# Kernel optimization log

Hardware: AMD Instinct MI355X
Metric: run time of the kernel (lower is better)

## Reference

```python
import jax, jax.numpy as jnp
import numpy as np

LOG_STD_MAX = 2.0
LOG_STD_MIN = -5.0
N_LAYERS = 10
HID = 512
OBS = 21
ACT = 8
OVERALL = HID * (N_LAYERS + 1)          # 5632
IN_DIM = OBS + OVERALL                   # 5653
OUT_DIM = OVERALL + ACT                  # 5640
BATCH = 8192


def _block_banded_weight(rng):
    # staircase partitions, exactly as layer_init
    in_d = [0, OBS] + [OBS + HID * i for i in range(1, N_LAYERS + 2)]
    out_d = [0] + [HID * i for i in range(1, N_LAYERS + 2)] + [OUT_DIM]
    W = np.zeros((OUT_DIM, IN_DIM), dtype=np.float32)
    for i in range(N_LAYERS + 2):
        r0, r1 = out_d[i], out_d[i + 1]
        c0, c1 = in_d[i], in_d[i + 1]
        fan_in = c1 - c0
        std = np.sqrt(2.0 / fan_in)  # kaiming_normal_ fan_in, gain sqrt(2)
        W[r0:r1, c0:c1] = rng.standard_normal((r1 - r0, c1 - c0)).astype(np.float32) * std
    return jnp.asarray(W)


def setup_inputs() -> dict:
    key = jax.random.key(0)
    k1, k2, k3, k4, k5, k6 = jax.random.split(key, 6)
    rng = np.random.default_rng(0)
    return {
        "obs": jax.random.normal(k1, (BATCH, OBS), dtype=jnp.float32),
        "hidden0": jax.random.uniform(k2, (BATCH, OVERALL), dtype=jnp.float32),
        "prev_mean": jax.random.normal(k3, (BATCH, ACT), dtype=jnp.float32),
        "prev_logstd": jax.random.normal(k4, (BATCH, ACT), dtype=jnp.float32),
        "W_mean": _block_banded_weight(rng),
        "b_mean": jnp.zeros((OUT_DIM,), dtype=jnp.float32),
        "W_logstd": jax.random.normal(k5, (ACT, IN_DIM), dtype=jnp.float32) / np.sqrt(IN_DIM),
        "b_logstd": jax.random.normal(k6, (ACT,), dtype=jnp.float32) * 0.01,
    }


def reference(obs, hidden0, prev_mean, prev_logstd, W_mean, b_mean, W_logstd, b_logstd):
    x = jnp.concatenate([obs, hidden0], axis=1)            # [B, IN_DIM]
    new_x = x @ W_mean.T + b_mean                          # [B, OUT_DIM]
    new_hidden = jax.nn.relu(new_x[:, :-ACT])              # [B, OVERALL]
    new_mean = new_x[:, -ACT:]                             # [B, ACT]
    new_log_std = x @ W_logstd.T + b_logstd                # [B, ACT]
    # outputs come from the PREVIOUS step's (mean, log_std)
    log_std = jnp.tanh(prev_logstd)
    log_std = LOG_STD_MIN + 0.5 * (LOG_STD_MAX - LOG_STD_MIN) * (log_std + 1.0)
    return (prev_mean, log_std, new_hidden, new_mean, new_log_std)
```

## Files before the change

kernel.cpp:

```cpp
#include <hip/hip_runtime.h>
#include <math.h>

typedef unsigned short u16;
typedef unsigned int u32;
typedef __attribute__((ext_vector_type(8))) short short8;
typedef __attribute__((ext_vector_type(4))) float float4v;

#define BATCH   8192
#define OBS     21
#define HID     512
#define NL      10
#define OVERALL 5632
#define IN_DIM  5653
#define OUT_DIM 5640
#define ACT     8

#define O_PM   0
#define O_LS   65536
#define O_NH   131072
#define O_NM   (131072 + BATCH*OVERALL)
#define O_NLS  (O_NM + 65536)

#define WSP_TOTAL (10*512*512)
#define WSP_BYTES ((size_t)WSP_TOTAL * 2)

__device__ __forceinline__ u16 f2bf(float f) {
    u32 u = __float_as_uint(f);
    u32 r = (u + 0x7fffu + ((u >> 16) & 1u)) >> 16;
    return (u16)r;
}
__device__ __forceinline__ u32 pkbf(float a, float b) {
    return (u32)f2bf(a) | ((u32)f2bf(b) << 16);
}
__device__ __forceinline__ void gload_lds16(const void* g, void* l) {
    __builtin_amdgcn_global_load_lds(
        (const __attribute__((address_space(1))) char*)g,
        (__attribute__((address_space(3))) char*)l, 16, 0, 0);
}

__global__ __launch_bounds__(256) void k_pack(const float* __restrict__ Wm,
                                              u16* __restrict__ ws) {
    int idx = blockIdx.x * 256 + threadIdx.x;
    if (idx >= WSP_TOTAL) return;
    int z = idx >> 18;
    int rem = idx & 262143;
    int n = rem >> 9, k = rem & 511;
    float v = Wm[(size_t)(512 * (z + 1) + n) * IN_DIM + OBS + 512 * z + k];
    ws[idx] = f2bf(v);
}

#define BM 128
#define BN 128
#define BK 32
#define A_LD 40
__global__ __launch_bounds__(256, 2) void k_gemm(const float* __restrict__ X,
                                                 const float* __restrict__ Wm_raw,
                                                 const u16* __restrict__ Wp,
                                                 const float* __restrict__ b_mean,
                                                 float* __restrict__ out_h,
                                                 int packed) {
    __shared__ __attribute__((aligned(16))) u16 As[BM * A_LD];
    __shared__ __attribute__((aligned(16))) u16 Bs[BN * BK];
    int t = threadIdx.x;
    int wave = t >> 6, lane = t & 63;
    int quad = lane >> 4, r16 = lane & 15;
    int gm = blockIdx.x * BM;
    int gn = blockIdx.y * BN;
    int z = blockIdx.z;
    int wm = (wave >> 1) * 64;
    int wn = (wave & 1) * 64;
    int ar = t >> 1;
    int ah = t & 1;

    const float* Arow = X + (size_t)(gm + ar) * OVERALL + z * 512 + ah * 16;

    float4v acc[4][4];
#pragma unroll
    for (int i = 0; i < 4; i++)
#pragma unroll
        for (int j = 0; j < 4; j++) acc[i][j] = (float4v)0.f;

    for (int k0 = 0; k0 < 512; k0 += BK) {
        __syncthreads();
        {
            const float* ga = Arow + k0;
            float4 v0 = *(const float4*)(ga);
            float4 v1 = *(const float4*)(ga + 4);
            float4 v2 = *(const float4*)(ga + 8);
            float4 v3 = *(const float4*)(ga + 12);
            uint4 p0, p1;
            p0.x = pkbf(v0.x, v0.y); p0.y = pkbf(v0.z, v0.w);
            p0.z = pkbf(v1.x, v1.y); p0.w = pkbf(v1.z, v1.w);
            p1.x = pkbf(v2.x, v2.y); p1.y = pkbf(v2.z, v2.w);
            p1.z = pkbf(v3.x, v3.y); p1.w = pkbf(v3.z, v3.w);
            *(uint4*)&As[ar * A_LD + ah * 16] = p0;
            *(uint4*)&As[ar * A_LD + ah * 16 + 8] = p1;
        }
        if (packed) {
#pragma unroll
            for (int it = 0; it < 2; ++it) {
                int n = it * 64 + wave * 16 + (lane >> 2);
                int kk = (lane & 3) * 8;
                const u16* gb = Wp + (size_t)z * (512 * 512) + (size_t)(gn + n) * 512 + k0 + kk;
                gload_lds16(gb, (char*)Bs + it * 4096 + wave * 1024);
            }
        } else {
            int n = t >> 1, h = t & 1;
            const float* gb = Wm_raw + (size_t)(512 * (z + 1) + gn + n) * IN_DIM
                              + OBS + 512 * z + k0 + h * 16;
#pragma unroll
            for (int e = 0; e < 16; e += 2)
                *(u32*)&Bs[n * BK + h * 16 + e] = pkbf(gb[e], gb[e + 1]);
        }
        __syncthreads();

        short8 af[4], bf[4];
#pragma unroll
        for (int i = 0; i < 4; i++) {
            af[i] = *(const short8*)&As[(wm + i * 16 + r16) * A_LD + quad * 8];
            bf[i] = *(const short8*)&Bs[(wn + i * 16 + r16) * BK + quad * 8];
        }
#pragma unroll
        for (int i = 0; i < 4; i++)
#pragma unroll
            for (int j = 0; j < 4; j++)
                acc[i][j] = __builtin_amdgcn_mfma_f32_16x16x32_bf16(af[i], bf[j], acc[i][j], 0, 0, 0);
    }

    int colblock = 512 * (z + 1);
#pragma unroll
    for (int j = 0; j < 4; j++) {
        int n_loc = gn + wn + j * 16 + r16;
        float bias = b_mean[colblock + n_loc];
#pragma unroll
        for (int i = 0; i < 4; i++) {
            int m0 = gm + wm + i * 16 + quad * 4;
#pragma unroll
            for (int r = 0; r < 4; r++) {
                float v = acc[i][j][r] + bias;
                out_h[(size_t)(m0 + r) * OVERALL + colblock + n_loc] = fmaxf(v, 0.f);
            }
        }
    }
}

__global__ __launch_bounds__(256) void k_block0(const float* __restrict__ obs,
                                                const float* __restrict__ Wm,
                                                const float* __restrict__ b_mean,
                                                float* __restrict__ out_h) {
    __shared__ float obs_s[8 * OBS];
    int t = threadIdx.x;
    int b0 = blockIdx.x * 8;
    if (t < 8 * OBS) obs_s[t] = obs[(size_t)b0 * OBS + t];
    __syncthreads();
#pragma unroll
    for (int half = 0; half < 2; ++half) {
        int n = half * 256 + t;
        float w[OBS];
#pragma unroll
        for (int k = 0; k < OBS; k++) w[k] = Wm[(size_t)n * IN_DIM + k];
        float bias = b_mean[n];
#pragma unroll 2
        for (int r = 0; r < 8; r++) {
            float a = bias;
#pragma unroll
            for (int k = 0; k < OBS; k++) a += obs_s[r * OBS + k] * w[k];
            out_h[(size_t)(b0 + r) * OVERALL + n] = fmaxf(a, 0.f);
        }
    }
}

__global__ __launch_bounds__(256) void k_thin(const float* __restrict__ obs,
                                              const float* __restrict__ X,
                                              const float* __restrict__ Wm,
                                              const float* __restrict__ Wls,
                                              const float* __restrict__ b_mean,
                                              const float* __restrict__ b_logstd,
                                              float* __restrict__ out_mean,
                                              float* __restrict__ out_ls) {
    int t = threadIdx.x, wave = t >> 6, lane = t & 63;
    int b0 = (blockIdx.x * 4 + wave) * 4;

    float als[4][8], amn[4][8];
#pragma unroll
    for (int r = 0; r < 4; r++)
#pragma unroll
        for (int n = 0; n < 8; n++) { als[r][n] = 0.f; amn[r][n] = 0.f; }

    for (int j = 0; j < 22; j++) {
        int k = j * 256 + lane * 4;
        float x[4][4];
#pragma unroll
        for (int r = 0; r < 4; r++)
            *(float4*)x[r] = *(const float4*)(X + (size_t)(b0 + r) * OVERALL + k);
#pragma unroll
        for (int n = 0; n < 8; n++) {
            const float* wp = Wls + (size_t)n * IN_DIM + OBS + k;
            float w0 = wp[0], w1 = wp[1], w2 = wp[2], w3 = wp[3];
#pragma unroll
            for (int r = 0; r < 4; r++) {
                als[r][n] += x[r][0] * w0 + x[r][1] * w1 + x[r][2] * w2 + x[r][3] * w3;
            }
        }
        if (j >= 20) {
#pragma unroll
            for (int n = 0; n < 8; n++) {
                const float* wp = Wm + (size_t)(OVERALL + n) * IN_DIM + OBS + k;
                float w0 = wp[0], w1 = wp[1], w2 = wp[2], w3 = wp[3];
#pragma unroll
                for (int r = 0; r < 4; r++) {
                    amn[r][n] += x[r][0] * w0 + x[r][1] * w1 + x[r][2] * w2 + x[r][3] * w3;
                }
            }
        }
    }
    if (lane < OBS) {
#pragma unroll
        for (int r = 0; r < 4; r++) {
            float xo = obs[(size_t)(b0 + r) * OBS + lane];
#pragma unroll
            for (int n = 0; n < 8; n++)
                als[r][n] += xo * Wls[(size_t)n * IN_DIM + lane];
        }
    }
#pragma unroll
    for (int s = 1; s < 64; s <<= 1) {
#pragma unroll
        for (int r = 0; r < 4; r++)
#pragma unroll
            for (int n = 0; n < 8; n++) {
                als[r][n] += __shfl_xor(als[r][n], s, 64);
                amn[r][n] += __shfl_xor(amn[r][n], s, 64);
            }
    }
    if (lane == 0) {
#pragma unroll
        for (int r = 0; r < 4; r++)
#pragma unroll
            for (int n = 0; n < 8; n++) {
                out_ls[(size_t)(b0 + r) * ACT + n] = als[r][n] + b_logstd[n];
                out_mean[(size_t)(b0 + r) * ACT + n] = amn[r][n] + b_mean[OVERALL + n];
            }
    }
}

__global__ __launch_bounds__(256) void k_small(const float* __restrict__ pm,
                                               const float* __restrict__ pls,
                                               float* __restrict__ o0,
                                               float* __restrict__ o1) {
    int i = blockIdx.x * 256 + threadIdx.x;
    float4 a = *(const float4*)(pm + (size_t)i * 4);
    *(float4*)(o0 + (size_t)i * 4) = a;
    float4 b = *(const float4*)(pls + (size_t)i * 4);
    float4 o;
    o.x = -5.f + 3.5f * (tanhf(b.x) + 1.f);
    o.y = -5.f + 3.5f * (tanhf(b.y) + 1.f);
    o.z = -5.f + 3.5f * (tanhf(b.z) + 1.f);
    o.w = -5.f + 3.5f * (tanhf(b.w) + 1.f);
    *(float4*)(o1 + (size_t)i * 4) = o;
}

extern "C" void kernel_launch(void* const* d_in, const int* in_sizes, int n_in,
                              void* d_out, int out_size, void* d_ws, size_t ws_size,
                              hipStream_t stream) {
    const float* obs         = (const float*)d_in[0];
    const float* hidden0     = (const float*)d_in[1];
    const float* prev_mean   = (const float*)d_in[2];
    const float* prev_logstd = (const float*)d_in[3];
    const float* W_mean      = (const float*)d_in[4];
    const float* b_mean      = (const float*)d_in[5];
    const float* W_logstd    = (const float*)d_in[6];
    const float* b_logstd    = (const float*)d_in[7];

    float* out   = (float*)d_out;
    float* o_pm  = out + O_PM;
    float* o_ls  = out + O_LS;
    float* o_nh  = out + O_NH;
    float* o_nm  = out + O_NM;
    float* o_nls = out + O_NLS;
    u16*   ws    = (u16*)d_ws;

    int packed = (ws != nullptr && ws_size >= WSP_BYTES) ? 1 : 0;

    if (packed) {
        k_pack<<<(WSP_TOTAL + 255) / 256, 256, 0, stream>>>(W_mean, ws);
    }
    k_gemm<<<dim3(BATCH / BM, 512 / BN, NL), 256, 0, stream>>>(
        hidden0, W_mean, ws, b_mean, o_nh, packed);
    k_block0<<<BATCH / 8, 256, 0, stream>>>(obs, W_mean, b_mean, o_nh);
    k_thin<<<BATCH / 16, 256, 0, stream>>>(obs, hidden0, W_mean, W_logstd,
                                           b_mean, b_logstd, o_nm, o_nls);
    k_small<<<64, 256, 0, stream>>>(prev_mean, prev_logstd, o_pm, o_ls);
}
```

Baseline: 512.5 us.

## Register-prefetch GEMM tiles, stage block0 and thin-kernel weights in LDS

The GEMM now loads the next K-slice of A and B into registers while the current slice is computed. B is staged through plain vector loads and LDS stores with a padded stride instead of direct global-to-LDS loads, and the occupancy hint is dropped. The block0 kernel caches the transposed first weight block in LDS and handles 32 rows per block with float4 stores. The thin kernel double-buffers bf16-converted logstd and mean weights in LDS. This reduces redundant global weight reads, but adds per-block weight-staging work and rounds the thin-kernel weights to bf16, which costs some precision.

```diff
diff --git a/kernel.cpp b/kernel.cpp
--- a/kernel.cpp
+++ b/kernel.cpp
@@ -32,10 +32,11 @@
 __device__ __forceinline__ u32 pkbf(float a, float b) {
     return (u32)f2bf(a) | ((u32)f2bf(b) << 16);
 }
-__device__ __forceinline__ void gload_lds16(const void* g, void* l) {
-    __builtin_amdgcn_global_load_lds(
-        (const __attribute__((address_space(1))) char*)g,
-        (__attribute__((address_space(3))) char*)l, 16, 0, 0);
+__device__ __forceinline__ float bfu2f(u32 bits_lo) {
+    return __uint_as_float(bits_lo << 16);
+}
+__device__ __forceinline__ float bfu2f_hi(u32 v) {
+    return __uint_as_float(v & 0xffff0000u);
 }
 
 __global__ __launch_bounds__(256) void k_pack(const float* __restrict__ Wm,
@@ -52,15 +53,16 @@
 #define BM 128
 #define BN 128
 #define BK 32
-#define A_LD 40
-__global__ __launch_bounds__(256, 2) void k_gemm(const float* __restrict__ X,
-                                                 const float* __restrict__ Wm_raw,
-                                                 const u16* __restrict__ Wp,
-                                                 const float* __restrict__ b_mean,
-                                                 float* __restrict__ out_h,
-                                                 int packed) {
-    __shared__ __attribute__((aligned(16))) u16 As[BM * A_LD];
-    __shared__ __attribute__((aligned(16))) u16 Bs[BN * BK];
+#define LDA 40
+#define LDB 40
+__global__ __launch_bounds__(256) void k_gemm(const float* __restrict__ X,
+                                              const float* __restrict__ Wm_raw,
+                                              const u16* __restrict__ Wp,
+                                              const float* __restrict__ b_mean,
+                                              float* __restrict__ out_h,
+                                              int packed) {
+    __shared__ __attribute__((aligned(16))) u16 As[BM * LDA];
+    __shared__ __attribute__((aligned(16))) u16 Bs[BN * LDB];
     int t = threadIdx.x;
     int wave = t >> 6, lane = t & 63;
     int quad = lane >> 4, r16 = lane & 15;
@@ -72,7 +74,26 @@
     int ar = t >> 1;
     int ah = t & 1;
 
-    const float* Arow = X + (size_t)(gm + ar) * OVERALL + z * 512 + ah * 16;
+    const float* Aptr = X + (size_t)(gm + ar) * OVERALL + z * 512 + ah * 16;
+    const u16*   Bp   = Wp + (size_t)z * (512 * 512) + (size_t)(gn + ar) * 512 + ah * 16;
+    const float* Br   = Wm_raw + (size_t)(512 * (z + 1) + gn + ar) * IN_DIM
+                        + OBS + 512 * z + ah * 16;
+
+    float4 a0 = *(const float4*)(Aptr);
+    float4 a1 = *(const float4*)(Aptr + 4);
+    float4 a2 = *(const float4*)(Aptr + 8);
+    float4 a3 = *(const float4*)(Aptr + 12);
+    uint4 pb0, pb1;
+    float4 rb0, rb1, rb2, rb3;
+    if (packed) {
+        pb0 = *(const uint4*)(Bp);
+        pb1 = *(const uint4*)(Bp + 8);
+    } else {
+        rb0 = *(const float4*)(Br);
+        rb1 = *(const float4*)(Br + 4);
+        rb2 = *(const float4*)(Br + 8);
+        rb3 = *(const float4*)(Br + 12);
+    }
 
     float4v acc[4][4];
 #pragma unroll
@@ -83,48 +104,58 @@
     for (int k0 = 0; k0 < 512; k0 += BK) {
         __syncthreads();
         {
-            const float* ga = Arow + k0;
-            float4 v0 = *(const float4*)(ga);
-            float4 v1 = *(const float4*)(ga + 4);
-            float4 v2 = *(const float4*)(ga + 8);
-            float4 v3 = *(const float4*)(ga + 12);
-            uint4 p0, p1;
-            p0.x = pkbf(v0.x, v0.y); p0.y = pkbf(v0.z, v0.w);
-            p0.z = pkbf(v1.x, v1.y); p0.w = pkbf(v1.z, v1.w);
-            p1.x = pkbf(v2.x, v2.y); p1.y = pkbf(v2.z, v2.w);
-            p1.z = pkbf(v3.x, v3.y); p1.w = pkbf(v3.z, v3.w);
-            *(uint4*)&As[ar * A_LD + ah * 16] = p0;
-            *(uint4*)&As[ar * A_LD + ah * 16 + 8] = p1;
+            uint4 w0, w1;
+            w0.x = pkbf(a0.x, a0.y); w0.y = pkbf(a0.z, a0.w);
+            w0.z = pkbf(a1.x, a1.y); w0.w = pkbf(a1.z, a1.w);
+            w1.x = pkbf(a2.x, a2.y); w1.y = pkbf(a2.z, a2.w);
+            w1.z = pkbf(a3.x, a3.y); w1.w = pkbf(a3.z, a3.w);
+            *(uint4*)&As[ar * LDA + ah * 16] = w0;
+            *(uint4*)&As[ar * LDA + ah * 16 + 8] = w1;
         }
         if (packed) {
-#pragma unroll
-            for (int it = 0; it < 2; ++it) {
-                int n = it * 64 + wave * 16 + (lane >> 2);
-                int kk = (lane & 3) * 8;
-                const u16* gb = Wp + (size_t)z * (512 * 512) + (size_t)(gn + n) * 512 + k0 + kk;
-                gload_lds16(gb, (char*)Bs + it * 4096 + wave * 1024);
-            }
+            *(uint4*)&Bs[ar * LDB + ah * 16] = pb0;
+            *(uint4*)&Bs[ar * LDB + ah * 16 + 8] = pb1;
         } else {
-            int n = t >> 1, h = t & 1;
-            const float* gb = Wm_raw + (size_t)(512 * (z + 1) + gn + n) * IN_DIM
-                              + OBS + 512 * z + k0 + h * 16;
-#pragma unroll
-            for (int e = 0; e < 16; e += 2)
-                *(u32*)&Bs[n * BK + h * 16 + e] = pkbf(gb[e], gb[e + 1]);
+            uint4 q0, q1;
+            q0.x = pkbf(rb0.x, rb0.y); q0.y = pkbf(rb0.z, rb0.w);
+            q0.z = pkbf(rb1.x, rb1.y); q0.w = pkbf(rb1.z, rb1.w);
+            q1.x = pkbf(rb2.x, rb2.y); q1.y = pkbf(rb2.z, rb2.w);
+            q1.z = pkbf(rb3.x, rb3.y); q1.w = pkbf(rb3.z, rb3.w);
+            *(uint4*)&Bs[ar * LDB + ah * 16] = q0;
+            *(uint4*)&Bs[ar * LDB + ah * 16 + 8] = q1;
         }
         __syncthreads();
 
-        short8 af[4], bf[4];
+        if (k0 + BK < 512) {
+            const float* ga = Aptr + k0 + BK;
+            a0 = *(const float4*)(ga);
+            a1 = *(const float4*)(ga + 4);
+            a2 = *(const float4*)(ga + 8);
+            a3 = *(const float4*)(ga + 12);
+            if (packed) {
+                const u16* gb = Bp + k0 + BK;
+                pb0 = *(const uint4*)(gb);
+                pb1 = *(const uint4*)(gb + 8);
+            } else {
+                const float* gb = Br + k0 + BK;
+                rb0 = *(const float4*)(gb);
+                rb1 = *(const float4*)(gb + 4);
+                rb2 = *(const float4*)(gb + 8);
+                rb3 = *(const float4*)(gb + 12);
+            }
+        }
+
+        short8 af[4], bfr[4];
 #pragma unroll
         for (int i = 0; i < 4; i++) {
-            af[i] = *(const short8*)&As[(wm + i * 16 + r16) * A_LD + quad * 8];
-            bf[i] = *(const short8*)&Bs[(wn + i * 16 + r16) * BK + quad * 8];
+            af[i]  = *(const short8*)&As[(wm + i * 16 + r16) * LDA + quad * 8];
+            bfr[i] = *(const short8*)&Bs[(wn + i * 16 + r16) * LDB + quad * 8];
         }
 #pragma unroll
         for (int i = 0; i < 4; i++)
 #pragma unroll
             for (int j = 0; j < 4; j++)
-                acc[i][j] = __builtin_amdgcn_mfma_f32_16x16x32_bf16(af[i], bf[j], acc[i][j], 0, 0, 0);
+                acc[i][j] = __builtin_amdgcn_mfma_f32_16x16x32_bf16(af[i], bfr[j], acc[i][j], 0, 0, 0);
     }
 
     int colblock = 512 * (z + 1);
@@ -144,29 +175,42 @@
     }
 }
 
+#define B0_ROWS 32
 __global__ __launch_bounds__(256) void k_block0(const float* __restrict__ obs,
                                                 const float* __restrict__ Wm,
                                                 const float* __restrict__ b_mean,
                                                 float* __restrict__ out_h) {
-    __shared__ float obs_s[8 * OBS];
+    __shared__ float w0[OBS * 512];
+    __shared__ float bias_s[512];
+    __shared__ float obs_s[B0_ROWS * OBS];
     int t = threadIdx.x;
-    int b0 = blockIdx.x * 8;
-    if (t < 8 * OBS) obs_s[t] = obs[(size_t)b0 * OBS + t];
+    int b0 = blockIdx.x * B0_ROWS;
+    for (int i = t; i < OBS * 512; i += 256) {
+        int n = i / OBS, k = i - n * OBS;
+        w0[k * 512 + n] = Wm[(size_t)n * IN_DIM + k];
+    }
+    for (int i = t; i < 512; i += 256) bias_s[i] = b_mean[i];
+    for (int i = t; i < B0_ROWS * OBS; i += 256) obs_s[i] = obs[(size_t)b0 * OBS + i];
     __syncthreads();
-#pragma unroll
-    for (int half = 0; half < 2; ++half) {
-        int n = half * 256 + t;
-        float w[OBS];
-#pragma unroll
-        for (int k = 0; k < OBS; k++) w[k] = Wm[(size_t)n * IN_DIM + k];
-        float bias = b_mean[n];
-#pragma unroll 2
-        for (int r = 0; r < 8; r++) {
-            float a = bias;
-#pragma unroll
-            for (int k = 0; k < OBS; k++) a += obs_s[r * OBS + k] * w[k];
-            out_h[(size_t)(b0 + r) * OVERALL + n] = fmaxf(a, 0.f);
-        }
+
+    int n0 = (t & 127) * 4;
+    int rh = t >> 7;
+#pragma unroll 4
+    for (int r = 0; r < 16; r++) {
+        int row = rh * 16 + r;
+        float acc0 = bias_s[n0], acc1 = bias_s[n0 + 1];
+        float acc2 = bias_s[n0 + 2], acc3 = bias_s[n0 + 3];
+#pragma unroll
+        for (int k = 0; k < OBS; k++) {
+            float xo = obs_s[row * OBS + k];
+            const float* wr = &w0[k * 512 + n0];
+            acc0 += xo * wr[0]; acc1 += xo * wr[1];
+            acc2 += xo * wr[2]; acc3 += xo * wr[3];
+        }
+        float4 o;
+        o.x = fmaxf(acc0, 0.f); o.y = fmaxf(acc1, 0.f);
+        o.z = fmaxf(acc2, 0.f); o.w = fmaxf(acc3, 0.f);
+        *(float4*)&out_h[(size_t)(b0 + row) * OVERALL + n0] = o;
     }
 }
 
@@ -178,38 +222,60 @@
                                               const float* __restrict__ b_logstd,
                                               float* __restrict__ out_mean,
                                               float* __restrict__ out_ls) {
+    __shared__ u16 wc[2][8 * 512];
+    __shared__ u16 wm11[8 * 512];
     int t = threadIdx.x, wave = t >> 6, lane = t & 63;
     int b0 = (blockIdx.x * 4 + wave) * 4;
 
+    for (int i = t; i < 4096; i += 256) {
+        int n = i >> 9, k = i & 511;
+        wm11[i] = f2bf(Wm[(size_t)(OVERALL + n) * IN_DIM + OBS + 5120 + k]);
+        wc[0][i] = f2bf(Wls[(size_t)n * IN_DIM + OBS + k]);
+    }
+
     float als[4][8], amn[4][8];
 #pragma unroll
     for (int r = 0; r < 4; r++)
 #pragma unroll
         for (int n = 0; n < 8; n++) { als[r][n] = 0.f; amn[r][n] = 0.f; }
 
-    for (int j = 0; j < 22; j++) {
-        int k = j * 256 + lane * 4;
-        float x[4][4];
-#pragma unroll
-        for (int r = 0; r < 4; r++)
-            *(float4*)x[r] = *(const float4*)(X + (size_t)(b0 + r) * OVERALL + k);
-#pragma unroll
-        for (int n = 0; n < 8; n++) {
-            const float* wp = Wls + (size_t)n * IN_DIM + OBS + k;
-            float w0 = wp[0], w1 = wp[1], w2 = wp[2], w3 = wp[3];
-#pragma unroll
-            for (int r = 0; r < 4; r++) {
-                als[r][n] += x[r][0] * w0 + x[r][1] * w1 + x[r][2] * w2 + x[r][3] * w3;
-            }
-        }
-        if (j >= 20) {
+    for (int c = 0; c < 11; c++) {
+        int buf = c & 1;
+        __syncthreads();
+        if (c + 1 < 11) {
+            for (int i = t; i < 4096; i += 256) {
+                int n = i >> 9, k = i & 511;
+                wc[buf ^ 1][i] = f2bf(Wls[(size_t)n * IN_DIM + OBS + (c + 1) * 512 + k]);
+            }
+        }
+#pragma unroll
+        for (int jj = 0; jj < 2; jj++) {
+            int kloc = jj * 256 + lane * 4;
+            int k = c * 512 + kloc;
+            float x[4][4];
+#pragma unroll
+            for (int r = 0; r < 4; r++)
+                *(float4*)x[r] = *(const float4*)(X + (size_t)(b0 + r) * OVERALL + k);
 #pragma unroll
             for (int n = 0; n < 8; n++) {
-                const float* wp = Wm + (size_t)(OVERALL + n) * IN_DIM + OBS + k;
-                float w0 = wp[0], w1 = wp[1], w2 = wp[2], w3 = wp[3];
-#pragma unroll
-                for (int r = 0; r < 4; r++) {
-                    amn[r][n] += x[r][0] * w0 + x[r][1] * w1 + x[r][2] * w2 + x[r][3] * w3;
+                u32 v0 = *(const u32*)&wc[buf][n * 512 + kloc];
+                u32 v1 = *(const u32*)&wc[buf][n * 512 + kloc + 2];
+                float w0 = bfu2f(v0 & 0xffffu), w1 = bfu2f_hi(v0);
+                float w2 = bfu2f(v1 & 0xffffu), w3 = bfu2f_hi(v1);
+#pragma unroll
+                for (int r = 0; r < 4; r++)
+                    als[r][n] += x[r][0] * w0 + x[r][1] * w1 + x[r][2] * w2 + x[r][3] * w3;
+            }
+            if (c == 10) {
+#pragma unroll
+                for (int n = 0; n < 8; n++) {
+                    u32 v0 = *(const u32*)&wm11[n * 512 + kloc];
+                    u32 v1 = *(const u32*)&wm11[n * 512 + kloc + 2];
+                    float w0 = bfu2f(v0 & 0xffffu), w1 = bfu2f_hi(v0);
+                    float w2 = bfu2f(v1 & 0xffffu), w3 = bfu2f_hi(v1);
+#pragma unroll
+                    for (int r = 0; r < 4; r++)
+                        amn[r][n] += x[r][0] * w0 + x[r][1] * w1 + x[r][2] * w2 + x[r][3] * w3;
                 }
             }
         }
@@ -287,7 +353,7 @@
     }
     k_gemm<<<dim3(BATCH / BM, 512 / BN, NL), 256, 0, stream>>>(
         hidden0, W_mean, ws, b_mean, o_nh, packed);
-    k_block0<<<BATCH / 8, 256, 0, stream>>>(obs, W_mean, b_mean, o_nh);
+    k_block0<<<BATCH / B0_ROWS, 256, 0, stream>>>(obs, W_mean, b_mean, o_nh);
     k_thin<<<BATCH / 16, 256, 0, stream>>>(obs, hidden0, W_mean, W_logstd,
                                            b_mean, b_logstd, o_nm, o_nls);
     k_small<<<64, 256, 0, stream>>>(prev_mean, prev_logstd, o_pm, o_ls);
```

Result: slower. 536.2 us (+4.6%).
